# Optimization experiments

Hardware: AMD Instinct MI355X
Metric: run time of the kernel (lower is better)

Reference implementation:

```python
import jax, jax.numpy as jnp
import numpy as np

# BiDAF-style co-attention with memory_len=2. Dropout is inference-mode identity.

def setup_inputs() -> dict:
    key = jax.random.key(0)
    k1, k2, k3, k4, k5 = jax.random.split(key, 5)
    d = 1024
    inp = jax.random.normal(k1, (8, 4096, d), dtype=jnp.float32)
    mem = jax.random.normal(k2, (8, 2, d), dtype=jnp.float32)
    w_input = jax.random.normal(k3, (d,), dtype=jnp.float32) * (1.0 / np.sqrt(d))
    w_memory = jax.random.normal(k4, (d,), dtype=jnp.float32) * (1.0 / np.sqrt(d))
    dot_scale = jax.random.uniform(k5, (d,), dtype=jnp.float32, minval=0.0, maxval=1.0 / np.sqrt(d))
    return {"input": inp, "memory": mem, "w_input": w_input, "w_memory": w_memory, "dot_scale": dot_scale}


def reference(input, memory, w_input, w_memory, dot_scale):
    # input: [b, L, d]; memory: [b, M=2, d]
    input_dot = jnp.einsum('bld,d->bl', input, w_input)[..., None]        # [b, L, 1]
    memory_dot = jnp.einsum('bmd,d->bm', memory, w_memory)[:, None, :]    # [b, 1, M]
    cross_dot = jnp.einsum('bld,bmd->blm', input * dot_scale, memory)     # [b, L, M]
    att = input_dot + memory_dot + cross_dot                              # [b, L, M]
    weight_one = jax.nn.softmax(att, axis=-1)                             # [b, L, M]
    output_one = jnp.einsum('blm,bmd->bld', weight_one, memory)           # [b, L, d]
    weight_two = jax.nn.softmax(jnp.max(att, axis=-1), axis=-1)           # [b, L]
    output_two = jnp.einsum('bl,bld->bd', weight_two, input)[:, None, :]  # [b, 1, d]
    return jnp.concatenate([input, output_one, input * output_one, output_two * output_one], axis=-1)
```

## Files before the change

### kernel.cpp

```cpp
#include <hip/hip_runtime.h>
#include <stdint.h>


#define BB 8
#define LL 4096
#define DD 1024

__global__ __launch_bounds__(256) void kP(const float* __restrict__ mem,
                                          const float* __restrict__ w_in,
                                          const float* __restrict__ w_mem,
                                          const float* __restrict__ ds,
                                          float* __restrict__ cvec,
                                          float* __restrict__ mdot) {
    int bm = blockIdx.x;
    int t  = threadIdx.x;
    const float* mrow = mem + bm * DD;
    float partial = 0.f;
#pragma unroll
    for (int j = 0; j < 4; ++j) {
        int d = t * 4 + j;
        float m = mrow[d];
        cvec[bm * DD + d] = fmaf(ds[d], m, w_in[d]);
        partial = fmaf(m, w_mem[d], partial);
    }
    __shared__ float red[4];
    for (int off = 32; off; off >>= 1) partial += __shfl_down(partial, off);
    if ((t & 63) == 0) red[t >> 6] = partial;
    __syncthreads();
    if (t == 0) mdot[bm] = red[0] + red[1] + red[2] + red[3];
}

__global__ __launch_bounds__(256) void kA(const float* __restrict__ input,
                                          const float* __restrict__ cvec,
                                          const float* __restrict__ mdot,
                                          float* __restrict__ att) {
    int blk = blockIdx.x;
    int b = blk >> 6, chunk = blk & 63;
    int t = threadIdx.x;
    int wave = t >> 6, lane = t & 63;

    const float4* c0p = (const float4*)(cvec + (size_t)b * 2 * DD);
    const float4* c1p = (const float4*)(cvec + (size_t)b * 2 * DD + DD);
    float4 rc0[4], rc1[4];
#pragma unroll
    for (int k = 0; k < 4; ++k) { rc0[k] = c0p[lane + 64 * k]; rc1[k] = c1p[lane + 64 * k]; }
    float md0 = mdot[b * 2], md1 = mdot[b * 2 + 1];

    for (int r = 0; r < 16; ++r) {
        int l = chunk * 64 + wave * 16 + r;
        const float4* row = (const float4*)(input + (size_t)(b * LL + l) * DD);
        float a0 = 0.f, a1 = 0.f;
#pragma unroll
        for (int k = 0; k < 4; ++k) {
            float4 x = row[lane + 64 * k];
            a0 = fmaf(x.x, rc0[k].x, a0); a0 = fmaf(x.y, rc0[k].y, a0);
            a0 = fmaf(x.z, rc0[k].z, a0); a0 = fmaf(x.w, rc0[k].w, a0);
            a1 = fmaf(x.x, rc1[k].x, a1); a1 = fmaf(x.y, rc1[k].y, a1);
            a1 = fmaf(x.z, rc1[k].z, a1); a1 = fmaf(x.w, rc1[k].w, a1);
        }
        for (int off = 32; off; off >>= 1) { a0 += __shfl_down(a0, off); a1 += __shfl_down(a1, off); }
        if (lane == 0) {
            ((float2*)att)[(size_t)b * LL + l] = make_float2(a0 + md0, a1 + md1);
        }
    }
}

__global__ __launch_bounds__(256) void kB(const float* __restrict__ att,
                                          float* __restrict__ stats,
                                          float* __restrict__ out2u) {
    int b = blockIdx.x, t = threadIdx.x;
    const float2* a = (const float2*)att + (size_t)b * LL;
    float mv[16];
    float tmax = -1e30f;
#pragma unroll
    for (int j = 0; j < 16; ++j) {
        float2 v = a[j * 256 + t];
        mv[j] = fmaxf(v.x, v.y);
        tmax = fmaxf(tmax, mv[j]);
    }
    __shared__ float red[4];
    for (int off = 32; off; off >>= 1) tmax = fmaxf(tmax, __shfl_down(tmax, off));
    if ((t & 63) == 0) red[t >> 6] = tmax;
    __syncthreads();
    float bmax = fmaxf(fmaxf(red[0], red[1]), fmaxf(red[2], red[3]));
    float s = 0.f;
#pragma unroll
    for (int j = 0; j < 16; ++j) s += __expf(mv[j] - bmax);
    __syncthreads();
    for (int off = 32; off; off >>= 1) s += __shfl_down(s, off);
    if ((t & 63) == 0) red[t >> 6] = s;
    __syncthreads();
    if (t == 0) { stats[b * 2] = bmax; stats[b * 2 + 1] = 1.f / (red[0] + red[1] + red[2] + red[3]); }
    for (int j = t; j < DD; j += 256) out2u[b * DD + j] = 0.f;
}

__global__ __launch_bounds__(256) void kC(const float* __restrict__ input,
                                          const float* __restrict__ att,
                                          const float* __restrict__ stats,
                                          float* __restrict__ out2u) {
    int blk = blockIdx.x;
    int b = blk >> 6, chunk = blk & 63;
    int t = threadIdx.x;
    float bmax = stats[b * 2];
    const float2* a = (const float2*)att + (size_t)b * LL + chunk * 64;
    const float4* inp = (const float4*)(input + (size_t)(b * LL + chunk * 64) * DD);
    float4 acc = make_float4(0.f, 0.f, 0.f, 0.f);
    for (int r = 0; r < 64; ++r) {
        float2 v = a[r];
        float e = __expf(fmaxf(v.x, v.y) - bmax);
        float4 u = inp[(size_t)r * 256 + t];
        acc.x = fmaf(e, u.x, acc.x);
        acc.y = fmaf(e, u.y, acc.y);
        acc.z = fmaf(e, u.z, acc.z);
        acc.w = fmaf(e, u.w, acc.w);
    }
    float* dst = out2u + (size_t)b * DD + 4 * t;
    atomicAdd(dst + 0, acc.x);
    atomicAdd(dst + 1, acc.y);
    atomicAdd(dst + 2, acc.z);
    atomicAdd(dst + 3, acc.w);
}

__global__ __launch_bounds__(256) void kD(const float* __restrict__ input,
                                          const float* __restrict__ memory,
                                          const float* __restrict__ att,
                                          const float* __restrict__ stats,
                                          const float* __restrict__ out2u,
                                          float* __restrict__ out) {
    int blk = blockIdx.x;
    int b = blk >> 8, chunk = blk & 255;
    int t = threadIdx.x;
    float invZ = stats[b * 2 + 1];

    float4 m0 = ((const float4*)(memory + (size_t)b * 2 * DD))[t];
    float4 m1 = ((const float4*)(memory + (size_t)b * 2 * DD + DD))[t];
    float4 o2 = ((const float4*)(out2u + (size_t)b * DD))[t];
    o2.x *= invZ; o2.y *= invZ; o2.z *= invZ; o2.w *= invZ;

    const float2* attb = (const float2*)att + (size_t)b * LL + chunk * 16;
    for (int r = 0; r < 16; ++r) {
        int l = chunk * 16 + r;
        float2 v = attb[r];
        float w0 = 1.f / (1.f + __expf(v.y - v.x));
        float w1 = 1.f - w0;
        float4 x = ((const float4*)(input + (size_t)(b * LL + l) * DD))[t];
        float4 o1;
        o1.x = fmaf(w0, m0.x, w1 * m1.x);
        o1.y = fmaf(w0, m0.y, w1 * m1.y);
        o1.z = fmaf(w0, m0.z, w1 * m1.z);
        o1.w = fmaf(w0, m0.w, w1 * m1.w);

        float* orow = out + (size_t)(b * LL + l) * (4 * DD);
        ((float4*)orow)[t] = x;
        ((float4*)(orow + DD))[t] = o1;
        ((float4*)(orow + 2 * DD))[t] = make_float4(x.x * o1.x, x.y * o1.y,
                                                    x.z * o1.z, x.w * o1.w);
        ((float4*)(orow + 3 * DD))[t] = make_float4(o2.x * o1.x, o2.y * o1.y,
                                                    o2.z * o1.z, o2.w * o1.w);
    }
}

extern "C" void kernel_launch(void* const* d_in, const int* in_sizes, int n_in,
                              void* d_out, int out_size, void* d_ws, size_t ws_size,
                              hipStream_t stream) {
    const float* input  = (const float*)d_in[0];
    const float* memory = (const float*)d_in[1];
    const float* w_in   = (const float*)d_in[2];
    const float* w_mem  = (const float*)d_in[3];
    const float* ds     = (const float*)d_in[4];
    float* out = (float*)d_out;

    float* ws    = (float*)d_ws;
    float* cvec  = ws;
    float* mdot  = ws + 16384;
    float* stats = ws + 16400;
    float* att   = ws + 16416;
    float* out2u = ws + 81952;

    kP<<<16,   256, 0, stream>>>(memory, w_in, w_mem, ds, cvec, mdot);
    kA<<<512,  256, 0, stream>>>(input, cvec, mdot, att);
    kB<<<BB,   256, 0, stream>>>(att, stats, out2u);
    kC<<<512,  256, 0, stream>>>(input, att, stats, out2u);
    kD<<<2048, 256, 0, stream>>>(input, memory, att, stats, out2u, out);
}
```

Baseline: 670.5 us.

## Fuse attention scores, online softmax pooling and first output sections into one pass

The score kernel now also writes the input, output_one and input*output_one sections. It accumulates a per-block online-softmax weighted sum of input rows, so input is read from memory only once instead of three times. A small reduction kernel merges the per-block max, sum and accumulator partials into output_two, and a final kernel writes only the last output section. This trades extra registers and a partial-accumulator buffer for much less global read traffic.

```diff
diff --git a/kernel.cpp b/kernel.cpp
--- a/kernel.cpp
+++ b/kernel.cpp
@@ -5,6 +5,9 @@
 #define BB 8
 #define LL 4096
 #define DD 1024
+#define BPB 128
+#define RPB 32
+#define RPW 8
 
 __global__ __launch_bounds__(256) void kP(const float* __restrict__ mem,
                                           const float* __restrict__ w_in,
@@ -31,132 +34,176 @@
 }
 
 __global__ __launch_bounds__(256) void kA(const float* __restrict__ input,
+                                          const float* __restrict__ memory,
                                           const float* __restrict__ cvec,
                                           const float* __restrict__ mdot,
-                                          float* __restrict__ att) {
+                                          float* __restrict__ att,
+                                          float* __restrict__ pmax,
+                                          float* __restrict__ pz,
+                                          float* __restrict__ pacc,
+                                          float* __restrict__ out) {
     int blk = blockIdx.x;
-    int b = blk >> 6, chunk = blk & 63;
+    int b = blk >> 7, chunk = blk & 127;
     int t = threadIdx.x;
     int wave = t >> 6, lane = t & 63;
 
     const float4* c0p = (const float4*)(cvec + (size_t)b * 2 * DD);
-    const float4* c1p = (const float4*)(cvec + (size_t)b * 2 * DD + DD);
-    float4 rc0[4], rc1[4];
-#pragma unroll
-    for (int k = 0; k < 4; ++k) { rc0[k] = c0p[lane + 64 * k]; rc1[k] = c1p[lane + 64 * k]; }
+    const float4* c1p = c0p + DD / 4;
+    const float4* m0p = (const float4*)(memory + (size_t)b * 2 * DD);
+    const float4* m1p = m0p + DD / 4;
+    float4 rc0[4], rc1[4], rm0[4], rm1[4], acc[4];
+#pragma unroll
+    for (int k = 0; k < 4; ++k) {
+        rc0[k] = c0p[lane + 64 * k];
+        rc1[k] = c1p[lane + 64 * k];
+        rm0[k] = m0p[lane + 64 * k];
+        rm1[k] = m1p[lane + 64 * k];
+        acc[k] = make_float4(0.f, 0.f, 0.f, 0.f);
+    }
     float md0 = mdot[b * 2], md1 = mdot[b * 2 + 1];
-
-    for (int r = 0; r < 16; ++r) {
-        int l = chunk * 64 + wave * 16 + r;
+    float lmax = -1e30f, zsum = 0.f;
+
+    int l0 = chunk * RPB + wave * RPW;
+    for (int r = 0; r < RPW; ++r) {
+        int l = l0 + r;
         const float4* row = (const float4*)(input + (size_t)(b * LL + l) * DD);
+        float4 x[4];
+#pragma unroll
+        for (int k = 0; k < 4; ++k) x[k] = row[lane + 64 * k];
+
         float a0 = 0.f, a1 = 0.f;
 #pragma unroll
         for (int k = 0; k < 4; ++k) {
-            float4 x = row[lane + 64 * k];
-            a0 = fmaf(x.x, rc0[k].x, a0); a0 = fmaf(x.y, rc0[k].y, a0);
-            a0 = fmaf(x.z, rc0[k].z, a0); a0 = fmaf(x.w, rc0[k].w, a0);
-            a1 = fmaf(x.x, rc1[k].x, a1); a1 = fmaf(x.y, rc1[k].y, a1);
-            a1 = fmaf(x.z, rc1[k].z, a1); a1 = fmaf(x.w, rc1[k].w, a1);
-        }
-        for (int off = 32; off; off >>= 1) { a0 += __shfl_down(a0, off); a1 += __shfl_down(a1, off); }
-        if (lane == 0) {
-            ((float2*)att)[(size_t)b * LL + l] = make_float2(a0 + md0, a1 + md1);
-        }
-    }
-}
-
-__global__ __launch_bounds__(256) void kB(const float* __restrict__ att,
-                                          float* __restrict__ stats,
-                                          float* __restrict__ out2u) {
+            a0 = fmaf(x[k].x, rc0[k].x, a0); a0 = fmaf(x[k].y, rc0[k].y, a0);
+            a0 = fmaf(x[k].z, rc0[k].z, a0); a0 = fmaf(x[k].w, rc0[k].w, a0);
+            a1 = fmaf(x[k].x, rc1[k].x, a1); a1 = fmaf(x[k].y, rc1[k].y, a1);
+            a1 = fmaf(x[k].z, rc1[k].z, a1); a1 = fmaf(x[k].w, rc1[k].w, a1);
+        }
+        for (int off = 32; off; off >>= 1) {
+            a0 += __shfl_xor(a0, off);
+            a1 += __shfl_xor(a1, off);
+        }
+        a0 += md0; a1 += md1;
+        if (lane == 0) ((float2*)att)[(size_t)b * LL + l] = make_float2(a0, a1);
+
+        float w0 = 1.f / (1.f + __expf(a1 - a0));
+        float w1 = 1.f - w0;
+        float ml = fmaxf(a0, a1);
+
+        float e;
+        if (ml > lmax) {
+            float s = __expf(lmax - ml);
+            zsum *= s;
+#pragma unroll
+            for (int k = 0; k < 4; ++k) {
+                acc[k].x *= s; acc[k].y *= s; acc[k].z *= s; acc[k].w *= s;
+            }
+            lmax = ml;
+            e = 1.f;
+        } else {
+            e = __expf(ml - lmax);
+        }
+        zsum += e;
+
+        float* orow = out + (size_t)(b * LL + l) * (4 * DD);
+#pragma unroll
+        for (int k = 0; k < 4; ++k) {
+            float4 o1;
+            o1.x = fmaf(w0, rm0[k].x, w1 * rm1[k].x);
+            o1.y = fmaf(w0, rm0[k].y, w1 * rm1[k].y);
+            o1.z = fmaf(w0, rm0[k].z, w1 * rm1[k].z);
+            o1.w = fmaf(w0, rm0[k].w, w1 * rm1[k].w);
+            ((float4*)orow)[lane + 64 * k] = x[k];
+            ((float4*)(orow + DD))[lane + 64 * k] = o1;
+            ((float4*)(orow + 2 * DD))[lane + 64 * k] =
+                make_float4(x[k].x * o1.x, x[k].y * o1.y,
+                            x[k].z * o1.z, x[k].w * o1.w);
+            acc[k].x = fmaf(e, x[k].x, acc[k].x);
+            acc[k].y = fmaf(e, x[k].y, acc[k].y);
+            acc[k].z = fmaf(e, x[k].z, acc[k].z);
+            acc[k].w = fmaf(e, x[k].w, acc[k].w);
+        }
+    }
+
+    __shared__ float swm[4], swz[4];
+    __shared__ __align__(16) float sacc[DD];
+    if (lane == 0) { swm[wave] = lmax; swz[wave] = zsum; }
+    for (int j = t; j < DD; j += 256) sacc[j] = 0.f;
+    __syncthreads();
+    float bmax = fmaxf(fmaxf(swm[0], swm[1]), fmaxf(swm[2], swm[3]));
+    float f = __expf(lmax - bmax);
+#pragma unroll
+    for (int k = 0; k < 4; ++k) {
+        int idx = 4 * (lane + 64 * k);
+        atomicAdd(&sacc[idx + 0], f * acc[k].x);
+        atomicAdd(&sacc[idx + 1], f * acc[k].y);
+        atomicAdd(&sacc[idx + 2], f * acc[k].z);
+        atomicAdd(&sacc[idx + 3], f * acc[k].w);
+    }
+    __syncthreads();
+    if (t == 0) {
+        float bz = 0.f;
+#pragma unroll
+        for (int w = 0; w < 4; ++w) bz += swz[w] * __expf(swm[w] - bmax);
+        pmax[blk] = bmax;
+        pz[blk]   = bz;
+    }
+    ((float4*)(pacc + (size_t)blk * DD))[t] = ((const float4*)sacc)[t];
+}
+
+__global__ __launch_bounds__(256) void kB(const float* __restrict__ pmax,
+                                          const float* __restrict__ pz,
+                                          const float* __restrict__ pacc,
+                                          float* __restrict__ out2) {
     int b = blockIdx.x, t = threadIdx.x;
-    const float2* a = (const float2*)att + (size_t)b * LL;
-    float mv[16];
-    float tmax = -1e30f;
-#pragma unroll
-    for (int j = 0; j < 16; ++j) {
-        float2 v = a[j * 256 + t];
-        mv[j] = fmaxf(v.x, v.y);
-        tmax = fmaxf(tmax, mv[j]);
-    }
-    __shared__ float red[4];
-    for (int off = 32; off; off >>= 1) tmax = fmaxf(tmax, __shfl_down(tmax, off));
-    if ((t & 63) == 0) red[t >> 6] = tmax;
-    __syncthreads();
-    float bmax = fmaxf(fmaxf(red[0], red[1]), fmaxf(red[2], red[3]));
-    float s = 0.f;
-#pragma unroll
-    for (int j = 0; j < 16; ++j) s += __expf(mv[j] - bmax);
-    __syncthreads();
-    for (int off = 32; off; off >>= 1) s += __shfl_down(s, off);
-    if ((t & 63) == 0) red[t >> 6] = s;
-    __syncthreads();
-    if (t == 0) { stats[b * 2] = bmax; stats[b * 2 + 1] = 1.f / (red[0] + red[1] + red[2] + red[3]); }
-    for (int j = t; j < DD; j += 256) out2u[b * DD + j] = 0.f;
-}
-
-__global__ __launch_bounds__(256) void kC(const float* __restrict__ input,
+    __shared__ float se[BPB];
+    const float* pm = pmax + b * BPB;
+    const float* pzb = pz + b * BPB;
+    float m = -1e30f;
+    for (int i = 0; i < BPB; ++i) m = fmaxf(m, pm[i]);
+    if (t < BPB) se[t] = __expf(pm[t] - m);
+    __syncthreads();
+    float Z = 0.f;
+    for (int i = 0; i < BPB; ++i) Z = fmaf(pzb[i], se[i], Z);
+    float invZ = 1.f / Z;
+
+    const float4* P = (const float4*)pacc + (size_t)b * BPB * (DD / 4);
+    float4 a = make_float4(0.f, 0.f, 0.f, 0.f);
+    for (int i = 0; i < BPB; ++i) {
+        float e = se[i];
+        float4 v = P[(size_t)i * 256 + t];
+        a.x = fmaf(e, v.x, a.x);
+        a.y = fmaf(e, v.y, a.y);
+        a.z = fmaf(e, v.z, a.z);
+        a.w = fmaf(e, v.w, a.w);
+    }
+    a.x *= invZ; a.y *= invZ; a.z *= invZ; a.w *= invZ;
+    ((float4*)(out2 + (size_t)b * DD))[t] = a;
+}
+
+__global__ __launch_bounds__(256) void kE(const float* __restrict__ memory,
                                           const float* __restrict__ att,
-                                          const float* __restrict__ stats,
-                                          float* __restrict__ out2u) {
-    int blk = blockIdx.x;
-    int b = blk >> 6, chunk = blk & 63;
-    int t = threadIdx.x;
-    float bmax = stats[b * 2];
-    const float2* a = (const float2*)att + (size_t)b * LL + chunk * 64;
-    const float4* inp = (const float4*)(input + (size_t)(b * LL + chunk * 64) * DD);
-    float4 acc = make_float4(0.f, 0.f, 0.f, 0.f);
-    for (int r = 0; r < 64; ++r) {
-        float2 v = a[r];
-        float e = __expf(fmaxf(v.x, v.y) - bmax);
-        float4 u = inp[(size_t)r * 256 + t];
-        acc.x = fmaf(e, u.x, acc.x);
-        acc.y = fmaf(e, u.y, acc.y);
-        acc.z = fmaf(e, u.z, acc.z);
-        acc.w = fmaf(e, u.w, acc.w);
-    }
-    float* dst = out2u + (size_t)b * DD + 4 * t;
-    atomicAdd(dst + 0, acc.x);
-    atomicAdd(dst + 1, acc.y);
-    atomicAdd(dst + 2, acc.z);
-    atomicAdd(dst + 3, acc.w);
-}
-
-__global__ __launch_bounds__(256) void kD(const float* __restrict__ input,
-                                          const float* __restrict__ memory,
-                                          const float* __restrict__ att,
-                                          const float* __restrict__ stats,
-                                          const float* __restrict__ out2u,
+                                          const float* __restrict__ out2,
                                           float* __restrict__ out) {
     int blk = blockIdx.x;
     int b = blk >> 8, chunk = blk & 255;
     int t = threadIdx.x;
-    float invZ = stats[b * 2 + 1];
-
     float4 m0 = ((const float4*)(memory + (size_t)b * 2 * DD))[t];
     float4 m1 = ((const float4*)(memory + (size_t)b * 2 * DD + DD))[t];
-    float4 o2 = ((const float4*)(out2u + (size_t)b * DD))[t];
-    o2.x *= invZ; o2.y *= invZ; o2.z *= invZ; o2.w *= invZ;
-
+    float4 o2 = ((const float4*)(out2 + (size_t)b * DD))[t];
     const float2* attb = (const float2*)att + (size_t)b * LL + chunk * 16;
     for (int r = 0; r < 16; ++r) {
-        int l = chunk * 16 + r;
         float2 v = attb[r];
         float w0 = 1.f / (1.f + __expf(v.y - v.x));
         float w1 = 1.f - w0;
-        float4 x = ((const float4*)(input + (size_t)(b * LL + l) * DD))[t];
         float4 o1;
         o1.x = fmaf(w0, m0.x, w1 * m1.x);
         o1.y = fmaf(w0, m0.y, w1 * m1.y);
         o1.z = fmaf(w0, m0.z, w1 * m1.z);
         o1.w = fmaf(w0, m0.w, w1 * m1.w);
-
-        float* orow = out + (size_t)(b * LL + l) * (4 * DD);
-        ((float4*)orow)[t] = x;
-        ((float4*)(orow + DD))[t] = o1;
-        ((float4*)(orow + 2 * DD))[t] = make_float4(x.x * o1.x, x.y * o1.y,
-                                                    x.z * o1.z, x.w * o1.w);
-        ((float4*)(orow + 3 * DD))[t] = make_float4(o2.x * o1.x, o2.y * o1.y,
-                                                    o2.z * o1.z, o2.w * o1.w);
+        float* orow = out + (size_t)(b * LL + chunk * 16 + r) * (4 * DD) + 3 * DD;
+        ((float4*)orow)[t] = make_float4(o2.x * o1.x, o2.y * o1.y,
+                                         o2.z * o1.z, o2.w * o1.w);
     }
 }
 
@@ -173,13 +220,14 @@
     float* ws    = (float*)d_ws;
     float* cvec  = ws;
     float* mdot  = ws + 16384;
-    float* stats = ws + 16400;
-    float* att   = ws + 16416;
-    float* out2u = ws + 81952;
+    float* att   = ws + 16400;
+    float* pmax  = ws + 81936;
+    float* pz    = ws + 82960;
+    float* out2  = ws + 83984;
+    float* pacc  = ws + 92176;
 
     kP<<<16,   256, 0, stream>>>(memory, w_in, w_mem, ds, cvec, mdot);
-    kA<<<512,  256, 0, stream>>>(input, cvec, mdot, att);
-    kB<<<BB,   256, 0, stream>>>(att, stats, out2u);
-    kC<<<512,  256, 0, stream>>>(input, att, stats, out2u);
-    kD<<<2048, 256, 0, stream>>>(input, memory, att, stats, out2u, out);
-}
+    kA<<<1024, 256, 0, stream>>>(input, memory, cvec, mdot, att, pmax, pz, pacc, out);
+    kB<<<BB,   256, 0, stream>>>(pmax, pz, pacc, out2);
+    kE<<<2048, 256, 0, stream>>>(memory, att, out2, out);
+}
```

After: 691.6 us. +3.2%, slower.
